# Kernel tuning notes

Measured on AMD Instinct MI355X. Metric: run time of the kernel, lower is better.

The kernel has to match this reference:

```python
import jax, jax.numpy as jnp
import numpy as np

TOPK, ALPHA, BETA, EPS = 13, 1.0, 6.0, 1e-9


def _make_boxes(key, shape, img=640.0):
    k1, k2 = jax.random.split(key)
    xy = jax.random.uniform(k1, shape[:-1] + (2,)) * (img - 80.0)
    wh = 10.0 + jax.random.uniform(k2, shape[:-1] + (2,)) * 70.0
    return jnp.concatenate([xy, xy + wh], axis=-1)


def setup_inputs() -> dict:
    key = jax.random.key(0)
    ks = jax.random.split(key, 8)
    B, L, C, n, K = 32, 8400, 1, 50, 17
    pred_scores = jax.random.uniform(ks[0], (B, L, C))
    pred_bboxes = _make_boxes(ks[1], (B, L, 4))
    pred_poses = jax.random.normal(ks[2], (B, L, K, 3))
    anchor_points = jax.random.uniform(ks[3], (L, 2)) * 640.0
    gt_labels = jax.random.randint(ks[4], (B, n, 1), 0, C)
    gt_bboxes = _make_boxes(ks[5], (B, n, 4))
    gt_poses = jax.random.normal(ks[6], (B, n, K, 3))
    pad_gt_mask = (jax.random.uniform(ks[7], (B, n, 1)) < 0.8).astype(jnp.float32)
    return dict(pred_scores=pred_scores, pred_bboxes=pred_bboxes, pred_poses=pred_poses,
                anchor_points=anchor_points, gt_labels=gt_labels, gt_bboxes=gt_bboxes,
                gt_poses=gt_poses, pad_gt_mask=pad_gt_mask, bg_index=1)


def _batch_iou(b1, b2):
    # b1: [B,n,4], b2: [B,L,4] (x1y1x2y2) -> [B,n,L]
    b1 = b1[:, :, None, :]
    b2 = b2[:, None, :, :]
    xy_min = jnp.maximum(b1[..., :2], b2[..., :2])
    xy_max = jnp.minimum(b1[..., 2:], b2[..., 2:])
    wh = jnp.clip(xy_max - xy_min, 0.0)
    inter = wh[..., 0] * wh[..., 1]
    a1 = (b1[..., 2] - b1[..., 0]) * (b1[..., 3] - b1[..., 1])
    a2 = (b2[..., 2] - b2[..., 0]) * (b2[..., 3] - b2[..., 1])
    union = a1 + a2 - inter
    return inter / (union + EPS)


def _points_in_boxes(points, bboxes):
    # points [L,2], bboxes [B,n,4] -> float [B,n,L]
    xy = points[None, None, :, :]                    # [1,1,L,2]
    lt = xy - bboxes[:, :, None, :2]                 # x - x1, y - y1
    rb = bboxes[:, :, None, 2:] - xy                 # x2 - x, y2 - y
    delta = jnp.concatenate([lt, rb], axis=-1)       # [B,n,L,4]
    return (delta.min(axis=-1) > EPS).astype(bboxes.dtype)


def _gather_topk(metrics, topk, topk_mask):
    # metrics [B,n,L], topk_mask [B,n,1] -> one-hot-per-gt topk mask [B,n,L]
    B, n, L = metrics.shape
    _, idxs = jax.lax.top_k(metrics, topk)           # [B,n,k]
    mask = jnp.broadcast_to(topk_mask > 0, idxs.shape)
    idxs = jnp.where(mask, idxs, 0)
    flat = jnp.zeros((B * n, L), metrics.dtype)
    flat = flat.at[jnp.arange(B * n)[:, None], idxs.reshape(B * n, topk)].add(1.0)
    is_in_topk = flat.reshape(B, n, L)
    # entries hit more than once (collisions from masked idx=0) are dropped, as in torch
    return jnp.where(is_in_topk > 1, 0.0, is_in_topk)


def reference(pred_scores, pred_bboxes, pred_poses, anchor_points, gt_labels,
              gt_bboxes, gt_poses, pad_gt_mask, bg_index):
    B, L, C = pred_scores.shape
    n = gt_bboxes.shape[1]
    K = gt_poses.shape[2]

    ious = _batch_iou(gt_bboxes, pred_bboxes)                                  # [B,n,L]
    # class score of each gt's label at every anchor: [B,n,L]
    bbox_cls_scores = pred_scores.transpose(0, 2, 1)[jnp.arange(B)[:, None], gt_labels[..., 0]]
    align = (bbox_cls_scores ** ALPHA) * (ious ** BETA)
    is_in_gts = _points_in_boxes(anchor_points, gt_bboxes)
    is_in_topk = _gather_topk(align * is_in_gts, TOPK, pad_gt_mask)
    mask_pos = is_in_topk * is_in_gts * pad_gt_mask                            # [B,n,L]
    mps = mask_pos.sum(axis=-2)                                                # [B,L]

    # resolve anchors assigned to multiple gts by max IoU (no-op when none)
    is_max_iou = (ious.argmax(axis=-2)[:, None, :] == jnp.arange(n)[None, :, None]).astype(ious.dtype)
    mask_pos = jnp.where(mps[:, None, :] > 1, is_max_iou, mask_pos)
    mps = mask_pos.sum(axis=-2)

    agi = mask_pos.argmax(axis=-2)                                             # [B,L]
    agi_flat = agi + jnp.arange(B, dtype=agi.dtype)[:, None] * n
    assigned_labels = gt_labels.reshape(-1)[agi_flat]
    assigned_labels = jnp.where(mps > 0, assigned_labels, bg_index)
    assigned_bboxes = gt_bboxes.reshape(-1, 4)[agi_flat]                       # [B,L,4]
    assigned_poses = gt_poses.reshape(-1, K, 3)[agi_flat]                      # [B,L,K,3]

    keep = jnp.array([i for i in range(C + 1) if i != bg_index])
    assigned_scores = jax.nn.one_hot(assigned_labels, C + 1)[..., keep]        # [B,L,C]

    align = align * mask_pos
    max_metrics = align.max(axis=-1, keepdims=True)                            # [B,n,1]
    max_ious = (ious * mask_pos).max(axis=-1, keepdims=True)                   # [B,n,1]
    align = align / (max_metrics + EPS) * max_ious
    assigned_scores = assigned_scores * align.max(axis=-2)[..., None]
    return assigned_labels, assigned_bboxes, assigned_poses, assigned_scores, agi_flat
```

## Files before the change

kernel.cpp:

```cpp
#include <hip/hip_runtime.h>

constexpr int NB = 32;
constexpr int NL = 8400;
constexpr int NC = 1;
constexpr int NG = 50;
constexpr int NKP = 17;
constexpr int TOPK = 13;
constexpr int BLTOT = NB * NL;
constexpr int NROW = NB * NG;
constexpr int CAP = 1024;
constexpr int JBLK = (NL + 255) / 256;
constexpr float FEPS = 1e-9f;

__device__ __forceinline__ float iou_gp(const float4 g, const float4 p, float garea) {
    const float ix1 = fmaxf(g.x, p.x), iy1 = fmaxf(g.y, p.y);
    const float ix2 = fminf(g.z, p.z), iy2 = fminf(g.w, p.w);
    const float iw = fmaxf(ix2 - ix1, 0.f), ih = fmaxf(iy2 - iy1, 0.f);
    const float inter = iw * ih;
    const float parea = (p.z - p.x) * (p.w - p.y);
    return inter / (garea + parea - inter + FEPS);
}

__global__ __launch_bounds__(256) void ingts_kernel(
    const float* __restrict__ anchor_points, const float* __restrict__ gt_bboxes,
    const float* __restrict__ pad_gt_mask,
    unsigned long long* __restrict__ ingts, int* __restrict__ cand_cnt,
    int* __restrict__ cand)
{
    __shared__ float4 gbox[NG];
    __shared__ int gact[NG];
    const int b = blockIdx.x / JBLK;
    const int jb = (blockIdx.x % JBLK) * 256;
    if (threadIdx.x < NG) {
        gbox[threadIdx.x] = reinterpret_cast<const float4*>(gt_bboxes)[b * NG + threadIdx.x];
        gact[threadIdx.x] = pad_gt_mask[b * NG + threadIdx.x] > 0.f;
    }
    __syncthreads();
    const int j = jb + threadIdx.x;
    if (j >= NL) return;
    const float2 a = reinterpret_cast<const float2*>(anchor_points)[j];
    unsigned long long m = 0;
    for (int i = 0; i < NG; ++i) {
        const float4 g = gbox[i];
        const float din = fminf(fminf(a.x - g.x, a.y - g.y), fminf(g.z - a.x, g.w - a.y));
        if (din > FEPS) {
            m |= (1ull << i);
            if (gact[i]) {
                const int row = b * NG + i;
                const int slot = atomicAdd(&cand_cnt[row], 1);
                if (slot < CAP) cand[row * CAP + slot] = j;
            }
        }
    }
    ingts[b * NL + j] = m;
}

__global__ __launch_bounds__(256) void topk_claim_kernel(
    const float* __restrict__ pred_scores, const float* __restrict__ pred_bboxes,
    const int* __restrict__ gt_labels, const float* __restrict__ gt_bboxes,
    const float* __restrict__ pad_gt_mask,
    const unsigned long long* __restrict__ ingts, const int* __restrict__ cand_cnt,
    const int* __restrict__ cand, unsigned long long* __restrict__ claims)
{
    const int row = blockIdx.x * 4 + (threadIdx.x >> 6);
    const int lane = threadIdx.x & 63;
    if (row >= NROW) return;
    if (pad_gt_mask[row] <= 0.f) return;
    const int b = row / NG, i = row % NG;
    const float4 g = reinterpret_cast<const float4*>(gt_bboxes)[row];
    const float garea = (g.z - g.x) * (g.w - g.y);
    const int lab = gt_labels[row];
    const int cnt = min(cand_cnt[row], CAP);

    float v[16]; int jj[16];
    #pragma unroll
    for (int s = 0; s < 16; ++s) {
        float mv = -1.f; int mj = NL + lane;
        const int c = s * 64 + lane;
        if (c < cnt) {
            const int j = cand[row * CAP + c];
            const float4 p = reinterpret_cast<const float4*>(pred_bboxes)[b * NL + j];
            const float iou = iou_gp(g, p, garea);
            const float sc = pred_scores[(b * NL + j) * NC + lab];
            const float i2 = iou * iou;
            mv = sc * i2 * i2 * i2;
            mj = j;
        }
        v[s] = mv; jj[s] = mj;
    }

    int ct = 0;
    for (int t = 0; t < TOPK; ++t) {
        float bv = -1.f; int bj = 0x7fffffff;
        #pragma unroll
        for (int s = 0; s < 16; ++s)
            if (v[s] > bv || (v[s] == bv && jj[s] < bj)) { bv = v[s]; bj = jj[s]; }
        for (int off = 32; off; off >>= 1) {
            const float v2 = __shfl_xor(bv, off);
            const int   j2 = __shfl_xor(bj, off);
            if (v2 > bv || (v2 == bv && j2 < bj)) { bv = v2; bj = j2; }
        }
        if (bv <= 0.f) break;
        if (lane == 0) atomicOr(&claims[b * NL + bj], 1ull << i);
        ++ct;
        #pragma unroll
        for (int s = 0; s < 16; ++s) if (jj[s] == bj) v[s] = -1.f;
    }

    const int needed = TOPK - ct;
    if (needed > 0) {
        int zcum = 0;
        for (int base = 0; base < NL && zcum < needed; base += 64) {
            const int j = base + lane;
            bool zero = false, ing = false;
            if (j < NL) {
                ing = (ingts[b * NL + j] >> i) & 1ull;
                if (!ing) {
                    zero = true;
                } else {
                    const float4 p = reinterpret_cast<const float4*>(pred_bboxes)[b * NL + j];
                    const float iou = iou_gp(g, p, garea);
                    const float sc = pred_scores[(b * NL + j) * NC + lab];
                    const float i2 = iou * iou;
                    zero = (sc * i2 * i2 * i2 == 0.f);
                }
            }
            const unsigned long long bal = __ballot(zero);
            const int rank = zcum + __popcll(bal & ((1ull << lane) - 1ull));
            if (zero && ing && rank < needed)
                atomicOr(&claims[b * NL + j], 1ull << i);
            zcum += __popcll(bal);
        }
    }
}

__global__ __launch_bounds__(256) void resolve_kernel(
    const float* __restrict__ pred_scores, const float* __restrict__ pred_bboxes,
    const int* __restrict__ gt_labels, const float* __restrict__ gt_bboxes,
    const unsigned long long* __restrict__ claims,
    int* __restrict__ agi_arr, float* __restrict__ align_arr,
    unsigned* __restrict__ rma, unsigned* __restrict__ rmi)
{
    const int idx = blockIdx.x * 256 + threadIdx.x;
    if (idx >= BLTOT) return;
    const int b = idx / NL;
    const unsigned long long M = claims[idx];
    const int mps = __popcll(M);
    int agi = -1;
    float av = 0.f;
    if (mps >= 1) {
        const float4 p = reinterpret_cast<const float4*>(pred_bboxes)[idx];
        if (mps == 1) {
            agi = __builtin_ctzll(M);
        } else {
            float best = -1.f;
            for (int i = 0; i < NG; ++i) {
                const float4 g = reinterpret_cast<const float4*>(gt_bboxes)[b * NG + i];
                const float ga = (g.z - g.x) * (g.w - g.y);
                const float iou = iou_gp(g, p, ga);
                if (iou > best) { best = iou; agi = i; }
            }
        }
        const float4 g = reinterpret_cast<const float4*>(gt_bboxes)[b * NG + agi];
        const float ga = (g.z - g.x) * (g.w - g.y);
        const float iou = iou_gp(g, p, ga);
        const int lab = gt_labels[b * NG + agi];
        const float s = pred_scores[idx * NC + lab];
        const float i2 = iou * iou;
        av = s * i2 * i2 * i2;
        atomicMax(&rma[b * NG + agi], __float_as_uint(av));
        atomicMax(&rmi[b * NG + agi], __float_as_uint(iou));
    }
    agi_arr[idx] = agi;
    align_arr[idx] = av;
}

__global__ __launch_bounds__(256) void finalize_kernel(
    const int* __restrict__ gt_labels, const float* __restrict__ gt_bboxes,
    const int* __restrict__ agi_arr, const float* __restrict__ align_arr,
    const unsigned* __restrict__ rma, const unsigned* __restrict__ rmi,
    const int* __restrict__ bg_ptr, float* __restrict__ out)
{
    const int idx = blockIdx.x * 256 + threadIdx.x;
    if (idx >= BLTOT) return;
    const int b = idx / NL;
    const int agi = agi_arr[idx];
    const int ag = (agi < 0) ? 0 : agi;
    const int bg = *bg_ptr;
    const int lab = gt_labels[b * NG + ag];

    float* labels = out;
    float* bboxes = out + (size_t)BLTOT;
    float* scores = out + (size_t)56 * BLTOT;
    float* agif   = out + (size_t)57 * BLTOT;

    labels[idx] = (agi >= 0) ? (float)lab : (float)bg;
    reinterpret_cast<float4*>(bboxes)[idx] =
        reinterpret_cast<const float4*>(gt_bboxes)[b * NG + ag];
    agif[idx] = (float)(ag + b * NG);

    float sc = 0.f;
    if (agi >= 0 && lab != bg) {
        const float mm = __uint_as_float(rma[b * NG + agi]);
        const float mi = __uint_as_float(rmi[b * NG + agi]);
        sc = align_arr[idx] / (mm + FEPS) * mi;
    }
    scores[idx] = sc;
}

__global__ __launch_bounds__(256) void poses_kernel(
    const float* __restrict__ gt_poses, const int* __restrict__ agi_arr,
    float* __restrict__ out_poses)
{
    const int q = blockIdx.x * 256 + threadIdx.x;
    constexpr int NQ = BLTOT * NKP * 3 / 4;
    if (q >= NQ) return;
    const int e0 = q * 4;
    float4 o;
    #pragma unroll
    for (int c = 0; c < 4; ++c) {
        const int e = e0 + c;
        const int p = e / (NKP * 3);
        const int r = e - p * (NKP * 3);
        const int b = p / NL;
        int a = agi_arr[p]; if (a < 0) a = 0;
        (&o.x)[c] = gt_poses[(b * NG + a) * (NKP * 3) + r];
    }
    reinterpret_cast<float4*>(out_poses)[q] = o;
}

extern "C" void kernel_launch(void* const* d_in, const int* in_sizes, int n_in,
                              void* d_out, int out_size, void* d_ws, size_t ws_size,
                              hipStream_t stream)
{
    const float* pred_scores   = (const float*)d_in[0];
    const float* pred_bboxes   = (const float*)d_in[1];
    const float* anchor_points = (const float*)d_in[3];
    const int*   gt_labels     = (const int*)d_in[4];
    const float* gt_bboxes     = (const float*)d_in[5];
    const float* gt_poses      = (const float*)d_in[6];
    const float* pad_gt_mask   = (const float*)d_in[7];
    const int*   bg_ptr        = (const int*)d_in[8];

    char* w = (char*)d_ws;
    size_t off = 0;
    unsigned long long* claims = (unsigned long long*)(w + off); off += (size_t)BLTOT * 8;
    unsigned* rma = (unsigned*)(w + off); off += (size_t)NROW * 4 * 4;
    unsigned* rmi = (unsigned*)(w + off); off += (size_t)NROW * 4 * 4;
    int* cand_cnt = (int*)(w + off); off += (size_t)NROW * 4;
    const size_t zero_bytes = off;
    int*   agi_arr   = (int*)  (w + off); off += (size_t)BLTOT * 4;
    float* align_arr = (float*)(w + off); off += (size_t)BLTOT * 4;
    unsigned long long* ingts = (unsigned long long*)(w + off); off += (size_t)BLTOT * 8;
    int* cand = (int*)(w + off); off += (size_t)NROW * CAP * 4;

    hipMemsetAsync(d_ws, 0, zero_bytes, stream);

    ingts_kernel<<<NB * JBLK, 256, 0, stream>>>(
        anchor_points, gt_bboxes, pad_gt_mask, ingts, cand_cnt, cand);

    topk_claim_kernel<<<(NROW + 3) / 4, 256, 0, stream>>>(
        pred_scores, pred_bboxes, gt_labels, gt_bboxes, pad_gt_mask,
        ingts, cand_cnt, cand, claims);

    resolve_kernel<<<(BLTOT + 255) / 256, 256, 0, stream>>>(
        pred_scores, pred_bboxes, gt_labels, gt_bboxes, claims,
        agi_arr, align_arr, rma, rmi);

    finalize_kernel<<<(BLTOT + 255) / 256, 256, 0, stream>>>(
        gt_labels, gt_bboxes, agi_arr, align_arr, rma, rmi, bg_ptr,
        (float*)d_out);

    poses_kernel<<<(BLTOT * NKP * 3 / 4 + 255) / 256, 256, 0, stream>>>(
        gt_poses, agi_arr, (float*)d_out + (size_t)5 * BLTOT);
}
```

Measured before the change: 182.3 us.

## Fuse poses gather into finalize kernel and zero claims inside ingts kernel

```diff
diff --git a/kernel.cpp b/kernel.cpp
--- a/kernel.cpp
+++ b/kernel.cpp
@@ -12,6 +12,8 @@
 constexpr int JBLK = (NL + 255) / 256;
 constexpr float FEPS = 1e-9f;
 
+typedef float f32x4 __attribute__((ext_vector_type(4)));
+
 __device__ __forceinline__ float iou_gp(const float4 g, const float4 p, float garea) {
     const float ix1 = fmaxf(g.x, p.x), iy1 = fmaxf(g.y, p.y);
     const float ix2 = fminf(g.z, p.z), iy2 = fminf(g.w, p.w);
@@ -25,7 +27,7 @@
     const float* __restrict__ anchor_points, const float* __restrict__ gt_bboxes,
     const float* __restrict__ pad_gt_mask,
     unsigned long long* __restrict__ ingts, int* __restrict__ cand_cnt,
-    int* __restrict__ cand)
+    int* __restrict__ cand, unsigned long long* __restrict__ claims)
 {
     __shared__ float4 gbox[NG];
     __shared__ int gact[NG];
@@ -38,6 +40,7 @@
     __syncthreads();
     const int j = jb + threadIdx.x;
     if (j >= NL) return;
+    claims[b * NL + j] = 0ull;
     const float2 a = reinterpret_cast<const float2*>(anchor_points)[j];
     unsigned long long m = 0;
     for (int i = 0; i < NG; ++i) {
@@ -175,14 +178,14 @@
     align_arr[idx] = av;
 }
 
-__global__ __launch_bounds__(256) void finalize_kernel(
+__global__ __launch_bounds__(256) void final_kernel(
     const int* __restrict__ gt_labels, const float* __restrict__ gt_bboxes,
+    const float* __restrict__ gt_poses,
     const int* __restrict__ agi_arr, const float* __restrict__ align_arr,
     const unsigned* __restrict__ rma, const unsigned* __restrict__ rmi,
     const int* __restrict__ bg_ptr, float* __restrict__ out)
 {
     const int idx = blockIdx.x * 256 + threadIdx.x;
-    if (idx >= BLTOT) return;
     const int b = idx / NL;
     const int agi = agi_arr[idx];
     const int ag = (agi < 0) ? 0 : agi;
@@ -191,6 +194,7 @@
 
     float* labels = out;
     float* bboxes = out + (size_t)BLTOT;
+    float* poses  = out + (size_t)5 * BLTOT;
     float* scores = out + (size_t)56 * BLTOT;
     float* agif   = out + (size_t)57 * BLTOT;
 
@@ -206,27 +210,22 @@
         sc = align_arr[idx] / (mm + FEPS) * mi;
     }
     scores[idx] = sc;
-}
-
-__global__ __launch_bounds__(256) void poses_kernel(
-    const float* __restrict__ gt_poses, const int* __restrict__ agi_arr,
-    float* __restrict__ out_poses)
-{
-    const int q = blockIdx.x * 256 + threadIdx.x;
+
     constexpr int NQ = BLTOT * NKP * 3 / 4;
-    if (q >= NQ) return;
-    const int e0 = q * 4;
-    float4 o;
-    #pragma unroll
-    for (int c = 0; c < 4; ++c) {
-        const int e = e0 + c;
-        const int p = e / (NKP * 3);
-        const int r = e - p * (NKP * 3);
-        const int b = p / NL;
-        int a = agi_arr[p]; if (a < 0) a = 0;
-        (&o.x)[c] = gt_poses[(b * NG + a) * (NKP * 3) + r];
-    }
-    reinterpret_cast<float4*>(out_poses)[q] = o;
+    for (int q = idx; q < NQ; q += BLTOT) {
+        const int e0 = q * 4;
+        f32x4 o;
+        #pragma unroll
+        for (int c = 0; c < 4; ++c) {
+            const int e = e0 + c;
+            const int p = e / (NKP * 3);
+            const int r = e - p * (NKP * 3);
+            const int pb = p / NL;
+            int a = agi_arr[p]; if (a < 0) a = 0;
+            o[c] = gt_poses[(pb * NG + a) * (NKP * 3) + r];
+        }
+        __builtin_nontemporal_store(o, reinterpret_cast<f32x4*>(poses) + q);
+    }
 }
 
 extern "C" void kernel_launch(void* const* d_in, const int* in_sizes, int n_in,
@@ -244,20 +243,20 @@
 
     char* w = (char*)d_ws;
     size_t off = 0;
-    unsigned long long* claims = (unsigned long long*)(w + off); off += (size_t)BLTOT * 8;
-    unsigned* rma = (unsigned*)(w + off); off += (size_t)NROW * 4 * 4;
-    unsigned* rmi = (unsigned*)(w + off); off += (size_t)NROW * 4 * 4;
+    unsigned* rma = (unsigned*)(w + off); off += (size_t)NROW * 4;
+    unsigned* rmi = (unsigned*)(w + off); off += (size_t)NROW * 4;
     int* cand_cnt = (int*)(w + off); off += (size_t)NROW * 4;
     const size_t zero_bytes = off;
+    unsigned long long* claims = (unsigned long long*)(w + off); off += (size_t)BLTOT * 8;
     int*   agi_arr   = (int*)  (w + off); off += (size_t)BLTOT * 4;
     float* align_arr = (float*)(w + off); off += (size_t)BLTOT * 4;
     unsigned long long* ingts = (unsigned long long*)(w + off); off += (size_t)BLTOT * 8;
     int* cand = (int*)(w + off); off += (size_t)NROW * CAP * 4;
 
-    hipMemsetAsync(d_ws, 0, zero_bytes, stream);
+    (void)hipMemsetAsync(d_ws, 0, zero_bytes, stream);
 
     ingts_kernel<<<NB * JBLK, 256, 0, stream>>>(
-        anchor_points, gt_bboxes, pad_gt_mask, ingts, cand_cnt, cand);
+        anchor_points, gt_bboxes, pad_gt_mask, ingts, cand_cnt, cand, claims);
 
     topk_claim_kernel<<<(NROW + 3) / 4, 256, 0, stream>>>(
         pred_scores, pred_bboxes, gt_labels, gt_bboxes, pad_gt_mask,
@@ -267,10 +266,7 @@
         pred_scores, pred_bboxes, gt_labels, gt_bboxes, claims,
         agi_arr, align_arr, rma, rmi);
 
-    finalize_kernel<<<(BLTOT + 255) / 256, 256, 0, stream>>>(
-        gt_labels, gt_bboxes, agi_arr, align_arr, rma, rmi, bg_ptr,
+    final_kernel<<<BLTOT / 256, 256, 0, stream>>>(
+        gt_labels, gt_bboxes, gt_poses, agi_arr, align_arr, rma, rmi, bg_ptr,
         (float*)d_out);
-
-    poses_kernel<<<(BLTOT * NKP * 3 / 4 + 255) / 256, 256, 0, stream>>>(
-        gt_poses, agi_arr, (float*)d_out + (size_t)5 * BLTOT);
-}
+}
```

Result: no change. 179.6 us (-1.5%).
